# Kernel optimization log

Measured on AMD Instinct MI355X. Metric: run time of the kernel, lower is better.

Reference implementation:

```python
import jax, jax.numpy as jnp
import numpy as np

# Model dims (match init_kwargs)
B, S, H = 1, 2048, 1024
E = 16            # n_routed_experts
I = 768           # moe_intermediate_size
TOPK = 4          # num_experts_per_tok
G = 4             # n_group
TOPK_G = 2        # topk_group
SCALE = 2.5       # routed_scaling_factor
N_SHARED = 1      # n_shared_experts


def setup_inputs() -> dict:
    key = jax.random.key(0)
    ks = jax.random.split(key, 9)
    def rn(k, shape, scale=0.02):
        return jax.random.normal(k, shape, dtype=jnp.float32) * scale
    return dict(
        hidden_states=jax.random.normal(ks[0], (B, S, H), dtype=jnp.float32),
        gate_w=rn(ks[1], (E, H)),
        gate_bias=jax.random.normal(ks[2], (E,), dtype=jnp.float32) * 0.1,
        w1=rn(ks[3], (E, I, H)),   # gate_proj weights [out,in]
        w2=rn(ks[4], (E, H, I)),   # down_proj weights
        w3=rn(ks[5], (E, I, H)),   # up_proj weights
        ws1=rn(ks[6], (I * N_SHARED, H)),
        ws2=rn(ks[7], (H, I * N_SHARED)),
        ws3=rn(ks[8], (I * N_SHARED, H)),
    )


def _route(x, gate_w, gate_bias):
    """noaux_tc routing: sigmoid scores + bias, group top-k, top_k experts."""
    n = x.shape[0]
    logits = jnp.einsum('nh,eh->ne', x.astype(jnp.float32), gate_w)  # [N,E]
    scores = jax.nn.sigmoid(logits)
    sb = scores + gate_bias                                          # biased scores
    # group score = sum of top-2 biased scores in each group
    gs = sb.reshape(n, G, E // G)
    group_scores = jnp.sum(jax.lax.top_k(gs, 2)[0], axis=-1)         # [N,G]
    _, gidx = jax.lax.top_k(group_scores, TOPK_G)                    # [N,TOPK_G]
    gmask = jnp.sum(jax.nn.one_hot(gidx, G, dtype=sb.dtype), axis=1) # [N,G]
    emask = jnp.repeat(gmask, E // G, axis=-1)                       # [N,E]
    masked = jnp.where(emask > 0, sb, -jnp.inf)
    _, tidx = jax.lax.top_k(masked, TOPK)                            # [N,TOPK]
    w = jnp.take_along_axis(scores, tidx, axis=1)                    # unbiased weights
    w = w / (jnp.sum(w, axis=-1, keepdims=True) + 1e-20)             # norm_topk_prob
    return tidx, w * SCALE


def reference(hidden_states, gate_w, gate_bias, w1, w2, w3, ws1, ws2, ws3):
    b, s, h = hidden_states.shape
    x = hidden_states.reshape(-1, h)                                 # [N,H]
    tidx, tw = _route(x, gate_w, gate_bias)
    n = x.shape[0]
    # dense combine weights [N,E] (zero for unselected experts)
    combine = jnp.zeros((n, E), x.dtype).at[jnp.arange(n)[:, None], tidx].add(tw)
    # grouped SwiGLU experts (dense-over-experts reference form)
    g = jnp.einsum('nh,eih->nei', x, w1)
    u = jnp.einsum('nh,eih->nei', x, w3)
    hact = jax.nn.silu(g) * u * combine[:, :, None]
    y = jnp.einsum('nei,ehi->nh', hact, w2)
    # shared expert SwiGLU
    shared = jnp.einsum('ni,hi->nh', jax.nn.silu(x @ ws1.T) * (x @ ws3.T), ws2)
    return (y + shared).reshape(b, s, h)
```

## Files before the change

### kernel.cpp

```cpp
#include <hip/hip_runtime.h>
#include <hip/hip_bf16.h>
#include <math.h>

#define N_TOK 2048
#define H_DIM 1024
#define N_EXP 16
#define I_DIM 768
#define TOPK 4
#define SCALE 2.5f

#define GU_SLOTS 256
#define DN_SLOTS 192
#define GU_TAB (8 * GU_SLOTS)
#define DN_TAB (8 * DN_SLOTS)
#define GU_NY (I_DIM / 64)
#define DN_NY (H_DIM / 128)
#define MAX_GRP 832

typedef __attribute__((ext_vector_type(8))) short bf16x8;
typedef __attribute__((ext_vector_type(4))) float f32x4;

#define OFF_COUNTS   0
#define OFF_OFFSETS  128
#define OFF_WGU      256
#define OFF_WDN      (OFF_WGU + GU_TAB*4)
#define OFF_TOKIDS   (OFF_WDN + DN_TAB*4)
#define OFF_TOKW     (OFF_TOKIDS + N_EXP*N_TOK*4)
#define OFF_XB       (OFF_TOKW + N_EXP*N_TOK*4)
#define OFF_HACT     (OFF_XB + (size_t)N_TOK*H_DIM*2)
#define OFF_GWT      (OFF_HACT + (size_t)N_TOK*(TOPK+1)*I_DIM*2)

__device__ __forceinline__ ushort f2bf(float f) {
    union { __hip_bfloat16 h; ushort u; } cv;
    cv.h = __float2bfloat16(f);
    return cv.u;
}
__device__ __forceinline__ unsigned pack2(float lo, float hi) {
    return (unsigned)f2bf(lo) | ((unsigned)f2bf(hi) << 16);
}
__device__ __forceinline__ void async_copy16(const void* g, void* l) {
    __builtin_amdgcn_global_load_lds(
        (const __attribute__((address_space(1))) unsigned int*)g,
        (__attribute__((address_space(3))) unsigned int*)l, 16, 0, 0);
}

__global__ void k_xconv(const float* __restrict__ x, ushort* __restrict__ xb) {
    int i = blockIdx.x * 256 + threadIdx.x;
    float4 v = ((const float4*)x)[i];
    uint2 p;
    p.x = pack2(v.x, v.y);
    p.y = pack2(v.z, v.w);
    ((uint2*)xb)[i] = p;
}

__global__ void k_gwt(const float* __restrict__ gw, float* __restrict__ gwT) {
    int i = blockIdx.x * 256 + threadIdx.x;
    int k = i >> 4, e = i & 15;
    gwT[i] = gw[e * H_DIM + k];
}

__launch_bounds__(256)
__global__ void k_route(const float* __restrict__ x, const float* __restrict__ gwT,
                        const float* __restrict__ gb,
                        int* __restrict__ counts, int* __restrict__ tok_ids,
                        float* __restrict__ tok_w) {
    __shared__ float lgs[4][N_EXP + 1];
    int tid = threadIdx.x;
    int wv = tid >> 6, lane = tid & 63;
    int e = lane & 15, ks = lane >> 4;
    int n = blockIdx.x * 4 + wv;

    const float* xr = x + (size_t)n * H_DIM + ks * 256;
    const float* wr = gwT + ks * 256 * N_EXP + e;
    float a0 = 0.f, a1 = 0.f, a2 = 0.f, a3 = 0.f;
#pragma unroll 8
    for (int k = 0; k < 256; k += 4) {
        float4 xv = *(const float4*)(xr + k);
        a0 += xv.x * wr[(k + 0) * N_EXP];
        a1 += xv.y * wr[(k + 1) * N_EXP];
        a2 += xv.z * wr[(k + 2) * N_EXP];
        a3 += xv.w * wr[(k + 3) * N_EXP];
    }
    float acc = (a0 + a1) + (a2 + a3);
    acc += __shfl_xor(acc, 16);
    acc += __shfl_xor(acc, 32);
    if (lane < 16) lgs[wv][lane] = acc;
    __syncthreads();

    if (tid < 4) {
        int n2 = blockIdx.x * 4 + tid;
        float sc[N_EXP], sb[N_EXP];
        for (int ee = 0; ee < N_EXP; ee++) {
            float l = lgs[tid][ee];
            sc[ee] = 1.f / (1.f + expf(-l));
            sb[ee] = sc[ee] + gb[ee];
        }
        float gsc[4];
        for (int g = 0; g < 4; g++) {
            float m1 = -1e30f, m2 = -1e30f;
            for (int j = 0; j < 4; j++) {
                float v = sb[4 * g + j];
                if (v > m1) { m2 = m1; m1 = v; }
                else if (v > m2) m2 = v;
            }
            gsc[g] = m1 + m2;
        }
        int g1 = 0;
        for (int g = 1; g < 4; g++) if (gsc[g] > gsc[g1]) g1 = g;
        int g2 = -1;
        for (int g = 0; g < 4; g++) {
            if (g == g1) continue;
            if (g2 < 0 || gsc[g] > gsc[g2]) g2 = g;
        }
        bool allowed[N_EXP];
        for (int ee = 0; ee < N_EXP; ee++) {
            int grp = ee >> 2;
            allowed[ee] = (grp == g1) || (grp == g2);
        }
        int chosen[TOPK];
        float wsum = 0.f;
        for (int k = 0; k < TOPK; k++) {
            int best = -1;
            for (int ee = 0; ee < N_EXP; ee++) {
                if (!allowed[ee]) continue;
                if (best < 0 || sb[ee] > sb[best]) best = ee;
            }
            chosen[k] = best;
            allowed[best] = false;
            wsum += sc[best];
        }
        float inv = SCALE / (wsum + 1e-20f);
        for (int k = 0; k < TOPK; k++) {
            int ee = chosen[k];
            int p = atomicAdd(&counts[ee], 1);
            tok_ids[ee * N_TOK + p] = n2;
            tok_w[ee * N_TOK + p] = sc[ee] * inv;
        }
    }
}

__global__ void k_scan(const int* __restrict__ counts, int* __restrict__ offsets,
                       int* __restrict__ wgu, int* __restrict__ wdn) {
    __shared__ int nmt_s[20], gpe_s[20];
    __shared__ int geb[20], deb[20];
    __shared__ int gmeta[MAX_GRP];
    __shared__ int gslot[MAX_GRP];
    __shared__ int ngu_s, ntot_s;
    int tid = threadIdx.x;
    for (int i = tid; i < GU_TAB; i += 256) wgu[i] = -1;
    for (int i = tid; i < DN_TAB; i += 256) wdn[i] = -1;
    if (tid < 17) {
        int c = (tid == 16) ? N_TOK : counts[tid];
        int nm = (c + 127) >> 7;
        nmt_s[tid] = nm;
        gpe_s[tid] = (nm + 3) >> 2;
    }
    __syncthreads();
    if (tid == 0) {
        int off = 0;
        for (int e = 0; e < N_EXP; e++) { offsets[e] = off; off += counts[e]; }
        offsets[N_EXP] = off;
        int g = 0, d = 0;
        for (int e = 0; e <= N_EXP; e++) {
            geb[e] = g; g += GU_NY * gpe_s[e];
            deb[e] = d; d += DN_NY * gpe_s[e];
        }
        geb[N_EXP + 1] = g; deb[N_EXP + 1] = d;
        ngu_s = g; ntot_s = g + d;
    }
    __syncthreads();
    int ngu = ngu_s, ntot = ntot_s;
    for (int g = tid; g < ntot; g += 256) {
        bool gu = g < ngu;
        int r = gu ? g : g - ngu;
        const int* eb = gu ? geb : deb;
        int e = 0;
        while (eb[e + 1] <= r) e++;
        int rem = r - eb[e];
        int gp = gpe_s[e];
        int y = rem / gp, mc = rem - y * gp;
        int m0t = mc * 4;
        int size = nmt_s[e] - m0t; if (size > 4) size = 4;
        gmeta[g] = e | (m0t << 5) | (y << 9) | (size << 24);
    }
    __syncthreads();
    if (tid < 8) {
        int s = 0;
        for (int g = tid; g < ngu; g += 8) { gslot[g] = s; s += (gmeta[g] >> 24); }
    } else if (tid < 16) {
        int c = tid - 8, s = 0;
        for (int g = ngu + c; g < ntot; g += 8) { gslot[g] = s; s += (gmeta[g] >> 24); }
    }
    __syncthreads();
    int k = tid & 3;
    for (int g = tid >> 2; g < ntot; g += 64) {
        int p = gmeta[g];
        int size = (p >> 24);
        if (k >= size) continue;
        int desc = (p & 0x1FFF) + (k << 5);
        bool gu = g < ngu;
        int r = gu ? g : g - ngu;
        int idx = (r & 7) + 8 * (gslot[g] + k);
        if (gu) wgu[idx] = desc; else wdn[idx] = desc;
    }
}

__launch_bounds__(256, 2)
__global__ void k_gateup(const ushort* __restrict__ xb, const float* __restrict__ w1,
                         const float* __restrict__ w3, const float* __restrict__ ws1,
                         const float* __restrict__ ws3, const int* __restrict__ counts,
                         const int* __restrict__ offsets, const int* __restrict__ wgu,
                         const int* __restrict__ tok_ids, const float* __restrict__ tok_w,
                         ushort* __restrict__ hact) {
    int desc = wgu[blockIdx.x];
    if (desc < 0) return;
    int e = desc & 31;
    int m0 = ((desc >> 5) & 15) * 128;
    int i0 = ((desc >> 9) & 15) * 64;
    int Me = (e == N_EXP) ? N_TOK : counts[e];
    const float* W1 = (e == N_EXP) ? ws1 : w1 + (size_t)e * I_DIM * H_DIM;
    const float* W3 = (e == N_EXP) ? ws3 : w3 + (size_t)e * I_DIM * H_DIM;
    int base = offsets[e];

    __shared__ ushort As[2][128][64];
    __shared__ ushort Bs[2][128][64];
    __shared__ float tws[128];

    int tid = threadIdx.x;
    int wv = tid >> 6, lane = tid & 63;
    int seg = lane & 7, rsub = lane >> 3;
    int gch = (seg ^ rsub) * 8;

    if (tid < 128) {
        int r = m0 + tid;
        tws[tid] = (e == N_EXP) ? 1.f : ((r < Me) ? tok_w[e * N_TOK + r] : 0.f);
    }

    const ushort* aptr[4];
#pragma unroll
    for (int j = 0; j < 4; j++) {
        int gr = m0 + wv * 32 + j * 8 + rsub;
        int tok = (e == N_EXP) ? gr : ((gr < Me) ? tok_ids[e * N_TOK + gr] : 0);
        aptr[j] = xb + (size_t)tok * H_DIM + gch;
    }
    const float* bptrf[4];
#pragma unroll
    for (int j = 0; j < 4; j++) {
        int r = wv * 32 + j * 8 + rsub;
        const float* W = (r < 64) ? (W1 + (size_t)(i0 + r) * H_DIM)
                                  : (W3 + (size_t)(i0 + r - 64) * H_DIM);
        bptrf[j] = W + gch;
    }

    int quad = lane >> 4, lr = lane & 15, rx = lr & 7;
    f32x4 acc[2][8] = {};

    const int NK = H_DIM / 64;
    float4 bv0[4], bv1[4];
#pragma unroll
    for (int j = 0; j < 4; j++) async_copy16(aptr[j], &As[0][wv * 32 + j * 8][0]);
#pragma unroll
    for (int j = 0; j < 4; j++) {
        bv0[j] = *(const float4*)(bptrf[j]);
        bv1[j] = *(const float4*)(bptrf[j] + 4);
    }
#pragma unroll
    for (int j = 0; j < 4; j++) {
        uint4 p;
        p.x = pack2(bv0[j].x, bv0[j].y);
        p.y = pack2(bv0[j].z, bv0[j].w);
        p.z = pack2(bv1[j].x, bv1[j].y);
        p.w = pack2(bv1[j].z, bv1[j].w);
        *(uint4*)&Bs[0][wv * 32 + j * 8 + rsub][seg * 8] = p;
    }
#pragma unroll
    for (int j = 0; j < 4; j++) {
        bv0[j] = *(const float4*)(bptrf[j] + 64);
        bv1[j] = *(const float4*)(bptrf[j] + 68);
    }
    __syncthreads();

    int c = 0;
    for (int k = 0; k < NK; k++) {
        int off = (k + 1) * 64;
        if (k + 1 < NK) {
#pragma unroll
            for (int j = 0; j < 4; j++)
                async_copy16(aptr[j] + off, &As[c ^ 1][wv * 32 + j * 8][0]);
        }
#pragma unroll
        for (int ks = 0; ks < 2; ks++) {
            int co = ((ks * 4 + quad) ^ rx) * 8;
            bf16x8 a0 = *(const bf16x8*)&As[c][wv * 32 + lr][co];
            bf16x8 a1 = *(const bf16x8*)&As[c][wv * 32 + 16 + lr][co];
#pragma unroll
            for (int ni = 0; ni < 8; ni++) {
                bf16x8 bf = *(const bf16x8*)&Bs[c][ni * 16 + lr][co];
                acc[0][ni] = __builtin_amdgcn_mfma_f32_16x16x32_bf16(a0, bf, acc[0][ni], 0, 0, 0);
                acc[1][ni] = __builtin_amdgcn_mfma_f32_16x16x32_bf16(a1, bf, acc[1][ni], 0, 0, 0);
            }
        }
        if (k + 1 < NK) {
#pragma unroll
            for (int j = 0; j < 4; j++) {
                uint4 p;
                p.x = pack2(bv0[j].x, bv0[j].y);
                p.y = pack2(bv0[j].z, bv0[j].w);
                p.z = pack2(bv1[j].x, bv1[j].y);
                p.w = pack2(bv1[j].z, bv1[j].w);
                *(uint4*)&Bs[c ^ 1][wv * 32 + j * 8 + rsub][seg * 8] = p;
            }
            if (k + 2 < NK) {
#pragma unroll
                for (int j = 0; j < 4; j++) {
                    bv0[j] = *(const float4*)(bptrf[j] + off + 64);
                    bv1[j] = *(const float4*)(bptrf[j] + off + 68);
                }
            }
        }
        __syncthreads();
        c ^= 1;
    }

#pragma unroll
    for (int mi = 0; mi < 2; mi++) {
#pragma unroll
        for (int ni = 0; ni < 4; ni++) {
            f32x4 g = acc[mi][ni];
            f32x4 u = acc[mi][ni + 4];
#pragma unroll
            for (int rg = 0; rg < 4; rg++) {
                int ml = wv * 32 + mi * 16 + quad * 4 + rg;
                int row = m0 + ml;
                if (row < Me) {
                    float gg = g[rg], uu = u[rg];
                    float act = (gg / (1.f + expf(-gg))) * uu * tws[ml];
                    hact[(size_t)(base + row) * I_DIM + i0 + ni * 16 + lr] = f2bf(act);
                }
            }
        }
    }
}

__launch_bounds__(256, 2)
__global__ void k_down(const ushort* __restrict__ hact, const float* __restrict__ w2,
                       const float* __restrict__ ws2, const int* __restrict__ counts,
                       const int* __restrict__ offsets, const int* __restrict__ wdn,
                       const int* __restrict__ tok_ids, float* __restrict__ out) {
    int desc = wdn[blockIdx.x];
    if (desc < 0) return;
    int e = desc & 31;
    int m0 = ((desc >> 5) & 15) * 128;
    int h0 = ((desc >> 9) & 15) * 128;
    int Me = (e == N_EXP) ? N_TOK : counts[e];
    const float* W2 = (e == N_EXP) ? ws2 : w2 + (size_t)e * H_DIM * I_DIM;
    int base = offsets[e];

    __shared__ ushort As[2][128][64];
    __shared__ ushort Bs[2][128][64];
    __shared__ int toks[128];

    int tid = threadIdx.x;
    int wv = tid >> 6, lane = tid & 63;
    int seg = lane & 7, rsub = lane >> 3;
    int gch = (seg ^ rsub) * 8;

    if (tid < 128) {
        int r = m0 + tid;
        toks[tid] = (e == N_EXP) ? r : ((r < Me) ? tok_ids[e * N_TOK + r] : 0);
    }

    const ushort* aptr[4];
#pragma unroll
    for (int j = 0; j < 4; j++) {
        int row = wv * 32 + j * 8 + rsub;
        aptr[j] = hact + (size_t)(base + m0 + row) * I_DIM + gch;
    }
    const float* bptrf[4];
#pragma unroll
    for (int j = 0; j < 4; j++) {
        int r = wv * 32 + j * 8 + rsub;
        bptrf[j] = W2 + (size_t)(h0 + r) * I_DIM + gch;
    }

    int quad = lane >> 4, lr = lane & 15, rx = lr & 7;
    f32x4 acc[2][8] = {};

    const int NK = I_DIM / 64;
    float4 bv0[4], bv1[4];
#pragma unroll
    for (int j = 0; j < 4; j++) async_copy16(aptr[j], &As[0][wv * 32 + j * 8][0]);
#pragma unroll
    for (int j = 0; j < 4; j++) {
        bv0[j] = *(const float4*)(bptrf[j]);
        bv1[j] = *(const float4*)(bptrf[j] + 4);
    }
#pragma unroll
    for (int j = 0; j < 4; j++) {
        uint4 p;
        p.x = pack2(bv0[j].x, bv0[j].y);
        p.y = pack2(bv0[j].z, bv0[j].w);
        p.z = pack2(bv1[j].x, bv1[j].y);
        p.w = pack2(bv1[j].z, bv1[j].w);
        *(uint4*)&Bs[0][wv * 32 + j * 8 + rsub][seg * 8] = p;
    }
#pragma unroll
    for (int j = 0; j < 4; j++) {
        bv0[j] = *(const float4*)(bptrf[j] + 64);
        bv1[j] = *(const float4*)(bptrf[j] + 68);
    }
    __syncthreads();

    int c = 0;
    for (int k = 0; k < NK; k++) {
        int off = (k + 1) * 64;
        if (k + 1 < NK) {
#pragma unroll
            for (int j = 0; j < 4; j++)
                async_copy16(aptr[j] + off, &As[c ^ 1][wv * 32 + j * 8][0]);
        }
#pragma unroll
        for (int ks = 0; ks < 2; ks++) {
            int co = ((ks * 4 + quad) ^ rx) * 8;
            bf16x8 a0 = *(const bf16x8*)&As[c][wv * 32 + lr][co];
            bf16x8 a1 = *(const bf16x8*)&As[c][wv * 32 + 16 + lr][co];
#pragma unroll
            for (int ni = 0; ni < 8; ni++) {
                bf16x8 bf = *(const bf16x8*)&Bs[c][ni * 16 + lr][co];
                acc[0][ni] = __builtin_amdgcn_mfma_f32_16x16x32_bf16(a0, bf, acc[0][ni], 0, 0, 0);
                acc[1][ni] = __builtin_amdgcn_mfma_f32_16x16x32_bf16(a1, bf, acc[1][ni], 0, 0, 0);
            }
        }
        if (k + 1 < NK) {
#pragma unroll
            for (int j = 0; j < 4; j++) {
                uint4 p;
                p.x = pack2(bv0[j].x, bv0[j].y);
                p.y = pack2(bv0[j].z, bv0[j].w);
                p.z = pack2(bv1[j].x, bv1[j].y);
                p.w = pack2(bv1[j].z, bv1[j].w);
                *(uint4*)&Bs[c ^ 1][wv * 32 + j * 8 + rsub][seg * 8] = p;
            }
            if (k + 2 < NK) {
#pragma unroll
                for (int j = 0; j < 4; j++) {
                    bv0[j] = *(const float4*)(bptrf[j] + off + 64);
                    bv1[j] = *(const float4*)(bptrf[j] + off + 68);
                }
            }
        }
        __syncthreads();
        c ^= 1;
    }

#pragma unroll
    for (int mi = 0; mi < 2; mi++) {
#pragma unroll
        for (int ni = 0; ni < 8; ni++) {
#pragma unroll
            for (int rg = 0; rg < 4; rg++) {
                int ml = wv * 32 + mi * 16 + quad * 4 + rg;
                int row = m0 + ml;
                if (row < Me) {
                    int tok = toks[ml];
                    atomicAdd(&out[(size_t)tok * H_DIM + h0 + ni * 16 + lr],
                              acc[mi][ni][rg]);
                }
            }
        }
    }
}

extern "C" void kernel_launch(void* const* d_in, const int* in_sizes, int n_in,
                              void* d_out, int out_size, void* d_ws, size_t ws_size,
                              hipStream_t stream) {
    const float* x   = (const float*)d_in[0];
    const float* gw  = (const float*)d_in[1];
    const float* gb  = (const float*)d_in[2];
    const float* w1  = (const float*)d_in[3];
    const float* w2  = (const float*)d_in[4];
    const float* w3  = (const float*)d_in[5];
    const float* ws1 = (const float*)d_in[6];
    const float* ws2 = (const float*)d_in[7];
    const float* ws3 = (const float*)d_in[8];
    float* out = (float*)d_out;

    char* wsb = (char*)d_ws;
    int* counts   = (int*)(wsb + OFF_COUNTS);
    int* offsets  = (int*)(wsb + OFF_OFFSETS);
    int* wgu      = (int*)(wsb + OFF_WGU);
    int* wdn      = (int*)(wsb + OFF_WDN);
    int* tok_ids  = (int*)(wsb + OFF_TOKIDS);
    float* tok_w  = (float*)(wsb + OFF_TOKW);
    ushort* xb    = (ushort*)(wsb + OFF_XB);
    ushort* hact  = (ushort*)(wsb + OFF_HACT);
    float* gwT    = (float*)(wsb + OFF_GWT);

    hipMemsetAsync(wsb, 0, 128, stream);
    hipMemsetAsync(d_out, 0, (size_t)out_size * 4, stream);

    k_xconv<<<N_TOK * H_DIM / 4 / 256, 256, 0, stream>>>(x, xb);
    k_gwt<<<N_EXP * H_DIM / 256, 256, 0, stream>>>(gw, gwT);
    k_route<<<N_TOK / 4, 256, 0, stream>>>(x, gwT, gb, counts, tok_ids, tok_w);
    k_scan<<<1, 256, 0, stream>>>(counts, offsets, wgu, wdn);
    k_gateup<<<GU_TAB, 256, 0, stream>>>(xb, w1, w3, ws1, ws3, counts, offsets,
                                         wgu, tok_ids, tok_w, hact);
    k_down<<<DN_TAB, 256, 0, stream>>>(hact, w2, ws2, counts, offsets, wdn,
                                       tok_ids, out);
}
```

Measured before the change: 368.6 us.

## Fuse x bf16 conversion into routing and single-buffer GEMM LDS for occupancy

The standalone x-to-bf16 conversion kernel is removed, and the routing kernel now writes the bf16 copy of x while it already reads x for the gate logits. This drops one kernel launch and one extra pass over x. In both expert GEMM kernels the double-buffered LDS tiles become single-buffered, and launch bounds rise from 2 to 4 blocks per CU to get more occupancy. The cost is that the async A loads and B stores are no longer overlapped with the MFMA compute inside a block, so each K step waits at a barrier, and latency hiding now relies on other resident blocks.

```diff
diff --git a/kernel.cpp b/kernel.cpp
--- a/kernel.cpp
+++ b/kernel.cpp
@@ -44,15 +44,6 @@
         (__attribute__((address_space(3))) unsigned int*)l, 16, 0, 0);
 }
 
-__global__ void k_xconv(const float* __restrict__ x, ushort* __restrict__ xb) {
-    int i = blockIdx.x * 256 + threadIdx.x;
-    float4 v = ((const float4*)x)[i];
-    uint2 p;
-    p.x = pack2(v.x, v.y);
-    p.y = pack2(v.z, v.w);
-    ((uint2*)xb)[i] = p;
-}
-
 __global__ void k_gwt(const float* __restrict__ gw, float* __restrict__ gwT) {
     int i = blockIdx.x * 256 + threadIdx.x;
     int k = i >> 4, e = i & 15;
@@ -63,7 +54,7 @@
 __global__ void k_route(const float* __restrict__ x, const float* __restrict__ gwT,
                         const float* __restrict__ gb,
                         int* __restrict__ counts, int* __restrict__ tok_ids,
-                        float* __restrict__ tok_w) {
+                        float* __restrict__ tok_w, ushort* __restrict__ xb) {
     __shared__ float lgs[4][N_EXP + 1];
     int tid = threadIdx.x;
     int wv = tid >> 6, lane = tid & 63;
@@ -71,6 +62,7 @@
     int n = blockIdx.x * 4 + wv;
 
     const float* xr = x + (size_t)n * H_DIM + ks * 256;
+    ushort* xbr = xb + (size_t)n * H_DIM + ks * 256;
     const float* wr = gwT + ks * 256 * N_EXP + e;
     float a0 = 0.f, a1 = 0.f, a2 = 0.f, a3 = 0.f;
 #pragma unroll 8
@@ -80,6 +72,12 @@
         a1 += xv.y * wr[(k + 1) * N_EXP];
         a2 += xv.z * wr[(k + 2) * N_EXP];
         a3 += xv.w * wr[(k + 3) * N_EXP];
+        if (e == 0) {
+            uint2 p;
+            p.x = pack2(xv.x, xv.y);
+            p.y = pack2(xv.z, xv.w);
+            *(uint2*)(xbr + k) = p;
+        }
     }
     float acc = (a0 + a1) + (a2 + a3);
     acc += __shfl_xor(acc, 16);
@@ -205,7 +203,7 @@
     }
 }
 
-__launch_bounds__(256, 2)
+__launch_bounds__(256, 4)
 __global__ void k_gateup(const ushort* __restrict__ xb, const float* __restrict__ w1,
                          const float* __restrict__ w3, const float* __restrict__ ws1,
                          const float* __restrict__ ws3, const int* __restrict__ counts,
@@ -222,8 +220,8 @@
     const float* W3 = (e == N_EXP) ? ws3 : w3 + (size_t)e * I_DIM * H_DIM;
     int base = offsets[e];
 
-    __shared__ ushort As[2][128][64];
-    __shared__ ushort Bs[2][128][64];
+    __shared__ ushort As[128][64];
+    __shared__ ushort Bs[128][64];
     __shared__ float tws[128];
 
     int tid = threadIdx.x;
@@ -258,68 +256,44 @@
     const int NK = H_DIM / 64;
     float4 bv0[4], bv1[4];
 #pragma unroll
-    for (int j = 0; j < 4; j++) async_copy16(aptr[j], &As[0][wv * 32 + j * 8][0]);
-#pragma unroll
     for (int j = 0; j < 4; j++) {
         bv0[j] = *(const float4*)(bptrf[j]);
         bv1[j] = *(const float4*)(bptrf[j] + 4);
     }
-#pragma unroll
-    for (int j = 0; j < 4; j++) {
-        uint4 p;
-        p.x = pack2(bv0[j].x, bv0[j].y);
-        p.y = pack2(bv0[j].z, bv0[j].w);
-        p.z = pack2(bv1[j].x, bv1[j].y);
-        p.w = pack2(bv1[j].z, bv1[j].w);
-        *(uint4*)&Bs[0][wv * 32 + j * 8 + rsub][seg * 8] = p;
-    }
-#pragma unroll
-    for (int j = 0; j < 4; j++) {
-        bv0[j] = *(const float4*)(bptrf[j] + 64);
-        bv1[j] = *(const float4*)(bptrf[j] + 68);
-    }
-    __syncthreads();
-
-    int c = 0;
     for (int k = 0; k < NK; k++) {
-        int off = (k + 1) * 64;
+        int off = k * 64;
+#pragma unroll
+        for (int j = 0; j < 4; j++) async_copy16(aptr[j] + off, &As[wv * 32 + j * 8][0]);
+#pragma unroll
+        for (int j = 0; j < 4; j++) {
+            uint4 p;
+            p.x = pack2(bv0[j].x, bv0[j].y);
+            p.y = pack2(bv0[j].z, bv0[j].w);
+            p.z = pack2(bv1[j].x, bv1[j].y);
+            p.w = pack2(bv1[j].z, bv1[j].w);
+            *(uint4*)&Bs[wv * 32 + j * 8 + rsub][seg * 8] = p;
+        }
         if (k + 1 < NK) {
 #pragma unroll
-            for (int j = 0; j < 4; j++)
-                async_copy16(aptr[j] + off, &As[c ^ 1][wv * 32 + j * 8][0]);
-        }
+            for (int j = 0; j < 4; j++) {
+                bv0[j] = *(const float4*)(bptrf[j] + off + 64);
+                bv1[j] = *(const float4*)(bptrf[j] + off + 68);
+            }
+        }
+        __syncthreads();
 #pragma unroll
         for (int ks = 0; ks < 2; ks++) {
             int co = ((ks * 4 + quad) ^ rx) * 8;
-            bf16x8 a0 = *(const bf16x8*)&As[c][wv * 32 + lr][co];
-            bf16x8 a1 = *(const bf16x8*)&As[c][wv * 32 + 16 + lr][co];
+            bf16x8 a0 = *(const bf16x8*)&As[wv * 32 + lr][co];
+            bf16x8 a1 = *(const bf16x8*)&As[wv * 32 + 16 + lr][co];
 #pragma unroll
             for (int ni = 0; ni < 8; ni++) {
-                bf16x8 bf = *(const bf16x8*)&Bs[c][ni * 16 + lr][co];
+                bf16x8 bf = *(const bf16x8*)&Bs[ni * 16 + lr][co];
                 acc[0][ni] = __builtin_amdgcn_mfma_f32_16x16x32_bf16(a0, bf, acc[0][ni], 0, 0, 0);
                 acc[1][ni] = __builtin_amdgcn_mfma_f32_16x16x32_bf16(a1, bf, acc[1][ni], 0, 0, 0);
             }
         }
-        if (k + 1 < NK) {
-#pragma unroll
-            for (int j = 0; j < 4; j++) {
-                uint4 p;
-                p.x = pack2(bv0[j].x, bv0[j].y);
-                p.y = pack2(bv0[j].z, bv0[j].w);
-                p.z = pack2(bv1[j].x, bv1[j].y);
-                p.w = pack2(bv1[j].z, bv1[j].w);
-                *(uint4*)&Bs[c ^ 1][wv * 32 + j * 8 + rsub][seg * 8] = p;
-            }
-            if (k + 2 < NK) {
-#pragma unroll
-                for (int j = 0; j < 4; j++) {
-                    bv0[j] = *(const float4*)(bptrf[j] + off + 64);
-                    bv1[j] = *(const float4*)(bptrf[j] + off + 68);
-                }
-            }
-        }
         __syncthreads();
-        c ^= 1;
     }
 
 #pragma unroll
@@ -342,7 +316,7 @@
     }
 }
 
-__launch_bounds__(256, 2)
+__launch_bounds__(256, 4)
 __global__ void k_down(const ushort* __restrict__ hact, const float* __restrict__ w2,
                        const float* __restrict__ ws2, const int* __restrict__ counts,
                        const int* __restrict__ offsets, const int* __restrict__ wdn,
@@ -356,8 +330,8 @@
     const float* W2 = (e == N_EXP) ? ws2 : w2 + (size_t)e * H_DIM * I_DIM;
     int base = offsets[e];
 
-    __shared__ ushort As[2][128][64];
-    __shared__ ushort Bs[2][128][64];
+    __shared__ ushort As[128][64];
+    __shared__ ushort Bs[128][64];
     __shared__ int toks[128];
 
     int tid = threadIdx.x;
@@ -389,68 +363,44 @@
     const int NK = I_DIM / 64;
     float4 bv0[4], bv1[4];
 #pragma unroll
-    for (int j = 0; j < 4; j++) async_copy16(aptr[j], &As[0][wv * 32 + j * 8][0]);
-#pragma unroll
     for (int j = 0; j < 4; j++) {
         bv0[j] = *(const float4*)(bptrf[j]);
         bv1[j] = *(const float4*)(bptrf[j] + 4);
     }
-#pragma unroll
-    for (int j = 0; j < 4; j++) {
-        uint4 p;
-        p.x = pack2(bv0[j].x, bv0[j].y);
-        p.y = pack2(bv0[j].z, bv0[j].w);
-        p.z = pack2(bv1[j].x, bv1[j].y);
-        p.w = pack2(bv1[j].z, bv1[j].w);
-        *(uint4*)&Bs[0][wv * 32 + j * 8 + rsub][seg * 8] = p;
-    }
-#pragma unroll
-    for (int j = 0; j < 4; j++) {
-        bv0[j] = *(const float4*)(bptrf[j] + 64);
-        bv1[j] = *(const float4*)(bptrf[j] + 68);
-    }
-    __syncthreads();
-
-    int c = 0;
     for (int k = 0; k < NK; k++) {
-        int off = (k + 1) * 64;
+        int off = k * 64;
+#pragma unroll
+        for (int j = 0; j < 4; j++) async_copy16(aptr[j] + off, &As[wv * 32 + j * 8][0]);
+#pragma unroll
+        for (int j = 0; j < 4; j++) {
+            uint4 p;
+            p.x = pack2(bv0[j].x, bv0[j].y);
+            p.y = pack2(bv0[j].z, bv0[j].w);
+            p.z = pack2(bv1[j].x, bv1[j].y);
+            p.w = pack2(bv1[j].z, bv1[j].w);
+            *(uint4*)&Bs[wv * 32 + j * 8 + rsub][seg * 8] = p;
+        }
         if (k + 1 < NK) {
 #pragma unroll
-            for (int j = 0; j < 4; j++)
-                async_copy16(aptr[j] + off, &As[c ^ 1][wv * 32 + j * 8][0]);
-        }
+            for (int j = 0; j < 4; j++) {
+                bv0[j] = *(const float4*)(bptrf[j] + off + 64);
+                bv1[j] = *(const float4*)(bptrf[j] + off + 68);
+            }
+        }
+        __syncthreads();
 #pragma unroll
         for (int ks = 0; ks < 2; ks++) {
             int co = ((ks * 4 + quad) ^ rx) * 8;
-            bf16x8 a0 = *(const bf16x8*)&As[c][wv * 32 + lr][co];
-            bf16x8 a1 = *(const bf16x8*)&As[c][wv * 32 + 16 + lr][co];
+            bf16x8 a0 = *(const bf16x8*)&As[wv * 32 + lr][co];
+            bf16x8 a1 = *(const bf16x8*)&As[wv * 32 + 16 + lr][co];
 #pragma unroll
             for (int ni = 0; ni < 8; ni++) {
-                bf16x8 bf = *(const bf16x8*)&Bs[c][ni * 16 + lr][co];
+                bf16x8 bf = *(const bf16x8*)&Bs[ni * 16 + lr][co];
                 acc[0][ni] = __builtin_amdgcn_mfma_f32_16x16x32_bf16(a0, bf, acc[0][ni], 0, 0, 0);
                 acc[1][ni] = __builtin_amdgcn_mfma_f32_16x16x32_bf16(a1, bf, acc[1][ni], 0, 0, 0);
             }
         }
-        if (k + 1 < NK) {
-#pragma unroll
-            for (int j = 0; j < 4; j++) {
-                uint4 p;
-                p.x = pack2(bv0[j].x, bv0[j].y);
-                p.y = pack2(bv0[j].z, bv0[j].w);
-                p.z = pack2(bv1[j].x, bv1[j].y);
-                p.w = pack2(bv1[j].z, bv1[j].w);
-                *(uint4*)&Bs[c ^ 1][wv * 32 + j * 8 + rsub][seg * 8] = p;
-            }
-            if (k + 2 < NK) {
-#pragma unroll
-                for (int j = 0; j < 4; j++) {
-                    bv0[j] = *(const float4*)(bptrf[j] + off + 64);
-                    bv1[j] = *(const float4*)(bptrf[j] + off + 68);
-                }
-            }
-        }
         __syncthreads();
-        c ^= 1;
     }
 
 #pragma unroll
@@ -499,9 +449,8 @@
     hipMemsetAsync(wsb, 0, 128, stream);
     hipMemsetAsync(d_out, 0, (size_t)out_size * 4, stream);
 
-    k_xconv<<<N_TOK * H_DIM / 4 / 256, 256, 0, stream>>>(x, xb);
     k_gwt<<<N_EXP * H_DIM / 256, 256, 0, stream>>>(gw, gwT);
-    k_route<<<N_TOK / 4, 256, 0, stream>>>(x, gwT, gb, counts, tok_ids, tok_w);
+    k_route<<<N_TOK / 4, 256, 0, stream>>>(x, gwT, gb, counts, tok_ids, tok_w, xb);
     k_scan<<<1, 256, 0, stream>>>(counts, offsets, wgu, wdn);
     k_gateup<<<GU_TAB, 256, 0, stream>>>(xb, w1, w3, ws1, ws3, counts, offsets,
                                          wgu, tok_ids, tok_w, hact);
```

Measured after the change: 369.7 us. About the same (+0.3%).
